# Kernel optimization log

Measured on AMD Instinct MI355X. Metric: run time of the kernel, lower is better.

The kernel has to match this reference:

```python
import jax, jax.numpy as jnp
import numpy as np
from jax.scipy.special import erfinv

N_CHUNKS = 64
D = 128          # input_dim
O = 256          # output_dim
B = 4096         # batch (batch_last)
P = D // 2       # number of 2D pairs

def get_borders_cdf_grid(n):
    # CDF (Gaussian-quantile) spaced grid borders; clip probs to keep endpoints finite
    p = jnp.clip(jnp.arange(n + 1, dtype=jnp.float32) / n, 0.5 / n, 1.0 - 0.5 / n)
    return jnp.sqrt(2.0) * erfinv(2.0 * p - 1.0)

BORDERS = get_borders_cdf_grid(N_CHUNKS)  # (n_chunks+1,)


def setup_inputs() -> dict:
    key = jax.random.key(0)
    ks = jax.random.split(key, 5)
    s = 1.0 / np.sqrt(D)
    return {
        "x": jax.random.normal(ks[0], (D, B), dtype=jnp.float32),
        "weight_lmKAN": jnp.ones((1,), dtype=jnp.float32),
        "apply_relu_linear": 1,
        "func_parameter": jax.random.uniform(ks[1], (N_CHUNKS + 1, N_CHUNKS + 1, O, P), minval=-s, maxval=s, dtype=jnp.float32),
        "scale_parameters": jnp.ones((D,), dtype=jnp.float32),
        "bias_parameters": jnp.zeros((D,), dtype=jnp.float32),
        "W_linear": jax.random.uniform(ks[2], (O, D), minval=-s, maxval=s, dtype=jnp.float32),
        "bias_linear": jax.random.uniform(ks[3], (O,), minval=-s, maxval=s, dtype=jnp.float32),
    }


def lmkan_2d(fp, x):
    """2D bucketized grid lookup + bilinear interpolation.
    fp: (G, G, O, P) with G = n_chunks+1; x: (D, B) -> out (O, B)."""
    n = fp.shape[0] - 1
    pairs = x.reshape(P, 2, -1)                      # adjacent-channel pairs
    eps = 1e-6
    x1 = jnp.clip(pairs[:, 0], BORDERS[0], BORDERS[-1] - eps)  # (P, B)
    x2 = jnp.clip(pairs[:, 1], BORDERS[0], BORDERS[-1] - eps)
    i = jnp.clip(jnp.searchsorted(BORDERS, x1, side='right') - 1, 0, n - 1)
    j = jnp.clip(jnp.searchsorted(BORDERS, x2, side='right') - 1, 0, n - 1)
    t1 = (x1 - BORDERS[i]) / (BORDERS[i + 1] - BORDERS[i])      # (P, B) in [0,1)
    t2 = (x2 - BORDERS[j]) / (BORDERS[j + 1] - BORDERS[j])
    pidx = jnp.arange(P)[:, None]                    # (P, 1) -> broadcasts to (P, B)

    def corner(ii, jj, w):
        g = fp[ii, jj, :, pidx]                      # gather -> (P, B, O)
        return jnp.einsum('pb,pbo->ob', w, g)

    return (corner(i,     j,     (1.0 - t1) * (1.0 - t2))
          + corner(i + 1, j,     t1 * (1.0 - t2))
          + corner(i,     j + 1, (1.0 - t1) * t2)
          + corner(i + 1, j + 1, t1 * t2))


def reference(x, weight_lmKAN, apply_relu_linear, func_parameter, scale_parameters, bias_parameters, W_linear, bias_linear):
    # relu_last=True branch of the original forward
    linear_out = W_linear @ x + bias_linear[:, None]         # (O, B)
    if apply_relu_linear:
        linear_out = jax.nn.relu(linear_out)
    xs = x * scale_parameters[:, None] + bias_parameters[:, None]  # apply_scale / apply_bias
    # apply_tanh=False
    lmkan_out = lmkan_2d(func_parameter, xs)                 # (O, B)
    return 1.0 * linear_out + weight_lmKAN * lmkan_out
```

## Files before the change

### kernel.cpp

```cpp
#include <hip/hip_runtime.h>
#include <hip/hip_fp16.h>


#define NB 4096
#define ND 128
#define NO 256
#define NP 64
#define NG 65
#define PANEL 16384
#define ROW2OFF (64 * 65 * 256)

typedef float f32x4 __attribute__((ext_vector_type(4)));
union Pack8 { __half h[8]; uint4 v; };

__device__ __forceinline__ int bsearch65(const float* B, float v) {
  int lo = 0, hi = 65;
  while (lo < hi) {
    int m = (lo + hi) >> 1;
    if (B[m] <= v) lo = m + 1; else hi = m;
  }
  int i = lo - 1;
  return i < 0 ? 0 : (i > 63 ? 63 : i);
}

__global__ __launch_bounds__(256) void lmkan_transpose2(
    const float* __restrict__ src, __half* __restrict__ dst) {
  const int panel = blockIdx.x;
  const int i = panel / NG, j = panel % NG;
  const int t = threadIdx.x;
  __shared__ __half lds[256 * 72];

  const f32x4* s4 = reinterpret_cast<const f32x4*>(src + (size_t)panel * PANEL);
#pragma unroll
  for (int k = 0; k < 16; ++k) {
    int idx4 = t + 256 * k;
    f32x4 v = __builtin_nontemporal_load(&s4[idx4]);
    int o = idx4 >> 4;
    int p0 = (idx4 & 15) * 4;
    union { __half2 h2[2]; uint2 u; } pk;
    pk.h2[0] = __floats2half2_rn(v[0], v[1]);
    pk.h2[1] = __floats2half2_rn(v[2], v[3]);
    *reinterpret_cast<uint2*>(&lds[o * 72 + p0]) = pk.u;
  }
  __syncthreads();

  const int p = t & 63, oc = t >> 6;
  __half* dbase = dst + (((size_t)(i * 64 + p) * NG + j) * NO) + oc * 64;
#pragma unroll
  for (int s = 0; s < 8; ++s) {
    Pack8 pk;
#pragma unroll
    for (int r = 0; r < 8; ++r) pk.h[r] = lds[(oc * 64 + 8 * s + r) * 72 + p];
    *reinterpret_cast<uint4*>(dbase + 8 * s) = pk.v;
  }
}

__device__ __forceinline__ void fma8(float acc[8], float w, uint4 v) {
  const __half2* h = reinterpret_cast<const __half2*>(&v);
#pragma unroll
  for (int k = 0; k < 4; ++k) {
    float2 f = __half22float2(h[k]);
    acc[2 * k]     = fmaf(w, f.x, acc[2 * k]);
    acc[2 * k + 1] = fmaf(w, f.y, acc[2 * k + 1]);
  }
}

__global__ __launch_bounds__(256) void lmkan_gather4(
    const float* __restrict__ x, const float* __restrict__ scale,
    const float* __restrict__ biasp, const float* __restrict__ wlm_p,
    const __half* __restrict__ fpt, float* __restrict__ out) {
  const int b = blockIdx.x;
  const int t = threadIdx.x;
  const int w = t >> 6;
  const int l = t & 63;
  const int sideJ = l >> 5;
  const int o0 = 8 * (l & 31);

  __shared__ float borders[66];
  __shared__ float xcol[ND];
  __shared__ int pbaseEl[NP];
  __shared__ float2 pws[2][NP];
  __shared__ float lm[4][NO];

  if (t < 65) {
    float pk = fminf(fmaxf((float)t * (1.0f / 64.0f), 0.0078125f), 0.9921875f);
    borders[t] = 1.41421356237309515f * erfinvf(2.0f * pk - 1.0f);
  }
  if (t < ND) xcol[t] = x[(size_t)t * NB + b];
  __syncthreads();

  if (t < NP) {
    const int p = t;
    float x1 = xcol[2 * p]     * scale[2 * p]     + biasp[2 * p];
    float x2 = xcol[2 * p + 1] * scale[2 * p + 1] + biasp[2 * p + 1];
    const float lo = borders[0];
    const float hi = borders[64] - 1e-6f;
    x1 = fminf(fmaxf(x1, lo), hi);
    x2 = fminf(fmaxf(x2, lo), hi);
    int i = bsearch65(borders, x1);
    int j = bsearch65(borders, x2);
    float t1 = (x1 - borders[i]) / (borders[i + 1] - borders[i]);
    float t2 = (x2 - borders[j]) / (borders[j + 1] - borders[j]);
    pbaseEl[p] = ((i * 64 + p) * NG + j) * NO;
    pws[0][p] = make_float2((1.0f - t1) * (1.0f - t2), t1 * (1.0f - t2));
    pws[1][p] = make_float2((1.0f - t1) * t2,          t1 * t2);
  }
  __syncthreads();

  float acc[8] = {0, 0, 0, 0, 0, 0, 0, 0};
  const int p0 = w * 16;
  const int loff = 8 * l;

  const __half* q = fpt + pbaseEl[p0] + loff;
  uint4 v0 = *reinterpret_cast<const uint4*>(q);
  uint4 v1 = *reinterpret_cast<const uint4*>(q + ROW2OFF);
#pragma unroll
  for (int pi = 0; pi < 16; ++pi) {
    const int p = p0 + pi;
    uint4 c0 = v0, c1 = v1;
    if (pi < 15) {
      const __half* qn = fpt + pbaseEl[p + 1] + loff;
      v0 = *reinterpret_cast<const uint4*>(qn);
      v1 = *reinterpret_cast<const uint4*>(qn + ROW2OFF);
    }
    const float2 wv = pws[sideJ][p];
    fma8(acc, wv.x, c0);
    fma8(acc, wv.y, c1);
  }
#pragma unroll
  for (int k = 0; k < 8; ++k) acc[k] += __shfl_xor(acc[k], 32, 64);
  if (l < 32) {
#pragma unroll
    for (int k = 0; k < 8; ++k) lm[w][o0 + k] = acc[k];
  }
  __syncthreads();

  const int o = t;
  float lmsum = lm[0][o] + lm[1][o] + lm[2][o] + lm[3][o];
  out[(size_t)o * NB + b] = wlm_p[0] * lmsum;
}

__global__ __launch_bounds__(256) void lmkan_linear(
    const float* __restrict__ x, const float* __restrict__ W,
    const float* __restrict__ bias_l, const int* __restrict__ relu_p,
    float* __restrict__ out) {
  const int b0 = blockIdx.x * 32;
  const int t = threadIdx.x;
  __shared__ __align__(16) float xs[32 * 132];

#pragma unroll
  for (int k = 0; k < 16; ++k) {
    int idx = t + 256 * k;
    int d = idx >> 5, bb = idx & 31;
    xs[bb * 132 + d] = x[(size_t)d * NB + b0 + bb];
  }
  __syncthreads();

  float acc[32];
#pragma unroll
  for (int bb = 0; bb < 32; ++bb) acc[bb] = 0.0f;

  const float4* W4 = reinterpret_cast<const float4*>(W + (size_t)t * ND);
#pragma unroll 8
  for (int d4 = 0; d4 < 32; ++d4) {
    float4 wv = W4[d4];
#pragma unroll
    for (int bb = 0; bb < 32; ++bb) {
      float4 xv = *reinterpret_cast<const float4*>(&xs[bb * 132 + d4 * 4]);
      acc[bb] = fmaf(wv.x, xv.x, acc[bb]);
      acc[bb] = fmaf(wv.y, xv.y, acc[bb]);
      acc[bb] = fmaf(wv.z, xv.z, acc[bb]);
      acc[bb] = fmaf(wv.w, xv.w, acc[bb]);
    }
  }

  const float bias = bias_l[t];
  const int rl = relu_p[0];
  float* orow = out + (size_t)t * NB + b0;
#pragma unroll
  for (int bb = 0; bb < 32; ++bb) {
    float v = acc[bb] + bias;
    if (rl) v = fmaxf(v, 0.0f);
    orow[bb] += v;
  }
}

__global__ __launch_bounds__(64) void lmkan_gather_direct(
    const float* __restrict__ x, const float* __restrict__ scale,
    const float* __restrict__ biasp, const float* __restrict__ W,
    const float* __restrict__ bias_l, const float* __restrict__ wlm_p,
    const int* __restrict__ relu_p, const float* __restrict__ fp,
    float* __restrict__ out) {
  const int b = blockIdx.x;
  const int t = threadIdx.x;

  __shared__ float borders[66];
  __shared__ __align__(16) float xcol[ND];
  __shared__ int pbase[NP];
  __shared__ float4 pw[NP];

  for (int k = t; k < 65; k += 64) {
    float pk = fminf(fmaxf((float)k * (1.0f / 64.0f), 0.0078125f), 0.9921875f);
    borders[k] = 1.41421356237309515f * erfinvf(2.0f * pk - 1.0f);
  }
  xcol[t]      = x[(size_t)t * NB + b];
  xcol[t + 64] = x[(size_t)(t + 64) * NB + b];
  __syncthreads();

  {
    const int p = t;
    float x1 = xcol[2 * p]     * scale[2 * p]     + biasp[2 * p];
    float x2 = xcol[2 * p + 1] * scale[2 * p + 1] + biasp[2 * p + 1];
    const float lo = borders[0];
    const float hi = borders[64] - 1e-6f;
    x1 = fminf(fmaxf(x1, lo), hi);
    x2 = fminf(fmaxf(x2, lo), hi);
    int i = bsearch65(borders, x1);
    int j = bsearch65(borders, x2);
    float t1 = (x1 - borders[i]) / (borders[i + 1] - borders[i]);
    float t2 = (x2 - borders[j]) / (borders[j + 1] - borders[j]);
    pbase[p] = i * NG + j;
    pw[p] = make_float4((1.0f - t1) * (1.0f - t2), t1 * (1.0f - t2),
                        (1.0f - t1) * t2, t1 * t2);
  }
  __syncthreads();

  float acc[4] = {0, 0, 0, 0};
  for (int p = 0; p < NP; ++p) {
    int base = pbase[p];
    float4 wv = pw[p];
#pragma unroll
    for (int k = 0; k < 4; ++k) {
      size_t r = ((size_t)base * NO + (4 * t + k)) * NP + p;
      acc[k] += wv.x * fp[r] + wv.y * fp[r + 65 * PANEL] +
                wv.z * fp[r + PANEL] + wv.w * fp[r + 66 * PANEL];
    }
  }

  const float wlm = wlm_p[0];
  const int rl = relu_p[0];
  const float4* xc4 = reinterpret_cast<const float4*>(xcol);
#pragma unroll
  for (int k = 0; k < 4; ++k) {
    const int o = 4 * t + k;
    const float4* wr = reinterpret_cast<const float4*>(W + (size_t)o * ND);
    float s = 0.0f;
#pragma unroll 8
    for (int d4 = 0; d4 < ND / 4; ++d4) {
      float4 wv = wr[d4];
      float4 xv = xc4[d4];
      s = fmaf(wv.x, xv.x, s);
      s = fmaf(wv.y, xv.y, s);
      s = fmaf(wv.z, xv.z, s);
      s = fmaf(wv.w, xv.w, s);
    }
    s += bias_l[o];
    if (rl) s = fmaxf(s, 0.0f);
    out[(size_t)o * NB + b] = s + wlm * acc[k];
  }
}

extern "C" void kernel_launch(void* const* d_in, const int* in_sizes, int n_in,
                              void* d_out, int out_size, void* d_ws, size_t ws_size,
                              hipStream_t stream) {
  const float* x     = reinterpret_cast<const float*>(d_in[0]);
  const float* wlm   = reinterpret_cast<const float*>(d_in[1]);
  const int*   relu  = reinterpret_cast<const int*>(d_in[2]);
  const float* fp    = reinterpret_cast<const float*>(d_in[3]);
  const float* scale = reinterpret_cast<const float*>(d_in[4]);
  const float* biasp = reinterpret_cast<const float*>(d_in[5]);
  const float* W     = reinterpret_cast<const float*>(d_in[6]);
  const float* bl    = reinterpret_cast<const float*>(d_in[7]);
  float* out = reinterpret_cast<float*>(d_out);

  const size_t need = (size_t)NG * NG * PANEL * sizeof(__half);
  if (ws_size >= need) {
    __half* fpt = reinterpret_cast<__half*>(d_ws);
    lmkan_transpose2<<<NG * NG, 256, 0, stream>>>(fp, fpt);
    lmkan_gather4<<<NB, 256, 0, stream>>>(x, scale, biasp, wlm, fpt, out);
    lmkan_linear<<<NB / 32, 256, 0, stream>>>(x, W, bl, relu, out);
  } else {
    lmkan_gather_direct<<<NB, 64, 0, stream>>>(x, scale, biasp, W, bl, wlm, relu, fp, out);
  }
}
```

Baseline: 193.6 us.

## Store transposed grid as [i][j][p][o] and gather four corners per lane

The half-precision workspace layout moves from [i][p][j][o] to [i][j][p][o], so each panel is written contiguously. The transpose kernel now writes full 512-byte rows per pair and uses an XOR swizzle on the LDS staging buffer to cut bank conflicts on the strided reads. In the gather kernel each lane now covers 4 outputs and loads all four bilinear corners (at offsets of 0, 1, 65 and 66 panels), which removes the cross-half shuffle reduction. In exchange it issues twice as many narrower 8-byte loads per pair, and the four corners sit in more widely separated memory regions.

Result: faster. 182.4 us (-5.8%).

```diff
diff --git a/kernel.cpp b/kernel.cpp
--- a/kernel.cpp
+++ b/kernel.cpp
@@ -8,7 +8,6 @@
 #define NP 64
 #define NG 65
 #define PANEL 16384
-#define ROW2OFF (64 * 65 * 256)
 
 typedef float f32x4 __attribute__((ext_vector_type(4)));
 union Pack8 { __half h[8]; uint4 v; };
@@ -23,10 +22,9 @@
   return i < 0 ? 0 : (i > 63 ? 63 : i);
 }
 
-__global__ __launch_bounds__(256) void lmkan_transpose2(
+__global__ __launch_bounds__(256) void lmkan_transpose3(
     const float* __restrict__ src, __half* __restrict__ dst) {
   const int panel = blockIdx.x;
-  const int i = panel / NG, j = panel % NG;
   const int t = threadIdx.x;
   __shared__ __half lds[256 * 72];
 
@@ -37,35 +35,40 @@
     f32x4 v = __builtin_nontemporal_load(&s4[idx4]);
     int o = idx4 >> 4;
     int p0 = (idx4 & 15) * 4;
+    int p0s = p0 ^ (((o >> 3) & 15) << 2);
     union { __half2 h2[2]; uint2 u; } pk;
     pk.h2[0] = __floats2half2_rn(v[0], v[1]);
     pk.h2[1] = __floats2half2_rn(v[2], v[3]);
-    *reinterpret_cast<uint2*>(&lds[o * 72 + p0]) = pk.u;
-  }
-  __syncthreads();
-
-  const int p = t & 63, oc = t >> 6;
-  __half* dbase = dst + (((size_t)(i * 64 + p) * NG + j) * NO) + oc * 64;
-#pragma unroll
-  for (int s = 0; s < 8; ++s) {
+    *reinterpret_cast<uint2*>(&lds[o * 72 + p0s]) = pk.u;
+  }
+  __syncthreads();
+
+  const int l = t & 63, w = t >> 6;
+  const int o0 = (l & 31) * 8;
+  const int swz = (l & 15) << 2;
+#pragma unroll
+  for (int ss = 0; ss < 8; ++ss) {
+    int p = ss * 8 + w * 2 + (l >> 5);
+    int prow = ((p & ~3) ^ swz) + (p & 3);
     Pack8 pk;
 #pragma unroll
-    for (int r = 0; r < 8; ++r) pk.h[r] = lds[(oc * 64 + 8 * s + r) * 72 + p];
-    *reinterpret_cast<uint4*>(dbase + 8 * s) = pk.v;
-  }
-}
-
-__device__ __forceinline__ void fma8(float acc[8], float w, uint4 v) {
-  const __half2* h = reinterpret_cast<const __half2*>(&v);
-#pragma unroll
-  for (int k = 0; k < 4; ++k) {
-    float2 f = __half22float2(h[k]);
-    acc[2 * k]     = fmaf(w, f.x, acc[2 * k]);
-    acc[2 * k + 1] = fmaf(w, f.y, acc[2 * k + 1]);
-  }
-}
-
-__global__ __launch_bounds__(256) void lmkan_gather4(
+    for (int r = 0; r < 8; ++r) pk.h[r] = lds[(o0 + r) * 72 + prow];
+    *reinterpret_cast<uint4*>(dst + ((size_t)panel * 64 + p) * NO + o0) = pk.v;
+  }
+}
+
+__device__ __forceinline__ void fma4h(float acc[4], float w, uint2 v) {
+  __half2 h0 = *reinterpret_cast<__half2*>(&v.x);
+  __half2 h1 = *reinterpret_cast<__half2*>(&v.y);
+  float2 f0 = __half22float2(h0);
+  float2 f1 = __half22float2(h1);
+  acc[0] = fmaf(w, f0.x, acc[0]);
+  acc[1] = fmaf(w, f0.y, acc[1]);
+  acc[2] = fmaf(w, f1.x, acc[2]);
+  acc[3] = fmaf(w, f1.y, acc[3]);
+}
+
+__global__ __launch_bounds__(256) void lmkan_gather5(
     const float* __restrict__ x, const float* __restrict__ scale,
     const float* __restrict__ biasp, const float* __restrict__ wlm_p,
     const __half* __restrict__ fpt, float* __restrict__ out) {
@@ -73,14 +76,12 @@
   const int t = threadIdx.x;
   const int w = t >> 6;
   const int l = t & 63;
-  const int sideJ = l >> 5;
-  const int o0 = 8 * (l & 31);
 
   __shared__ float borders[66];
   __shared__ float xcol[ND];
   __shared__ int pbaseEl[NP];
-  __shared__ float2 pws[2][NP];
-  __shared__ float lm[4][NO];
+  __shared__ float4 pw[NP];
+  __shared__ __align__(16) float lm[4][NO];
 
   if (t < 65) {
     float pk = fminf(fmaxf((float)t * (1.0f / 64.0f), 0.0078125f), 0.9921875f);
@@ -101,38 +102,42 @@
     int j = bsearch65(borders, x2);
     float t1 = (x1 - borders[i]) / (borders[i + 1] - borders[i]);
     float t2 = (x2 - borders[j]) / (borders[j + 1] - borders[j]);
-    pbaseEl[p] = ((i * 64 + p) * NG + j) * NO;
-    pws[0][p] = make_float2((1.0f - t1) * (1.0f - t2), t1 * (1.0f - t2));
-    pws[1][p] = make_float2((1.0f - t1) * t2,          t1 * t2);
-  }
-  __syncthreads();
-
-  float acc[8] = {0, 0, 0, 0, 0, 0, 0, 0};
+    pbaseEl[p] = ((i * NG + j) * 64 + p) * NO;
+    pw[p] = make_float4((1.0f - t1) * (1.0f - t2),
+                        (1.0f - t1) * t2,
+                        t1 * (1.0f - t2),
+                        t1 * t2);
+  }
+  __syncthreads();
+
+  float acc[4] = {0, 0, 0, 0};
   const int p0 = w * 16;
-  const int loff = 8 * l;
+  const int loff = 4 * l;
 
   const __half* q = fpt + pbaseEl[p0] + loff;
-  uint4 v0 = *reinterpret_cast<const uint4*>(q);
-  uint4 v1 = *reinterpret_cast<const uint4*>(q + ROW2OFF);
+  uint2 vA = *reinterpret_cast<const uint2*>(q);
+  uint2 vB = *reinterpret_cast<const uint2*>(q + PANEL);
+  uint2 vC = *reinterpret_cast<const uint2*>(q + 65 * PANEL);
+  uint2 vD = *reinterpret_cast<const uint2*>(q + 66 * PANEL);
 #pragma unroll
   for (int pi = 0; pi < 16; ++pi) {
     const int p = p0 + pi;
-    uint4 c0 = v0, c1 = v1;
+    uint2 cA = vA, cB = vB, cC = vC, cD = vD;
     if (pi < 15) {
       const __half* qn = fpt + pbaseEl[p + 1] + loff;
-      v0 = *reinterpret_cast<const uint4*>(qn);
-      v1 = *reinterpret_cast<const uint4*>(qn + ROW2OFF);
-    }
-    const float2 wv = pws[sideJ][p];
-    fma8(acc, wv.x, c0);
-    fma8(acc, wv.y, c1);
-  }
-#pragma unroll
-  for (int k = 0; k < 8; ++k) acc[k] += __shfl_xor(acc[k], 32, 64);
-  if (l < 32) {
-#pragma unroll
-    for (int k = 0; k < 8; ++k) lm[w][o0 + k] = acc[k];
-  }
+      vA = *reinterpret_cast<const uint2*>(qn);
+      vB = *reinterpret_cast<const uint2*>(qn + PANEL);
+      vC = *reinterpret_cast<const uint2*>(qn + 65 * PANEL);
+      vD = *reinterpret_cast<const uint2*>(qn + 66 * PANEL);
+    }
+    const float4 wv = pw[p];
+    fma4h(acc, wv.x, cA);
+    fma4h(acc, wv.y, cB);
+    fma4h(acc, wv.z, cC);
+    fma4h(acc, wv.w, cD);
+  }
+  *reinterpret_cast<float4*>(&lm[w][loff]) =
+      make_float4(acc[0], acc[1], acc[2], acc[3]);
   __syncthreads();
 
   const int o = t;
@@ -276,8 +281,8 @@
   const size_t need = (size_t)NG * NG * PANEL * sizeof(__half);
   if (ws_size >= need) {
     __half* fpt = reinterpret_cast<__half*>(d_ws);
-    lmkan_transpose2<<<NG * NG, 256, 0, stream>>>(fp, fpt);
-    lmkan_gather4<<<NB, 256, 0, stream>>>(x, scale, biasp, wlm, fpt, out);
+    lmkan_transpose3<<<NG * NG, 256, 0, stream>>>(fp, fpt);
+    lmkan_gather5<<<NB, 256, 0, stream>>>(x, scale, biasp, wlm, fpt, out);
     lmkan_linear<<<NB / 32, 256, 0, stream>>>(x, W, bl, relu, out);
   } else {
     lmkan_gather_direct<<<NB, 64, 0, stream>>>(x, scale, biasp, W, bl, wlm, relu, fp, out);
```

## Reorder fp16 table to pair-major slabs and swizzle transpose LDS

Applied to the files above, without the earlier changes.

The transposed fp16 parameter table changes from (i,p,j,o) ordering to a pair-major (p,i,j,o) layout. Each pair's data now sits in one contiguous slab, and the i+1 corner is a short NG*NO offset away instead of a far row offset. The transpose kernel also XOR-swizzles its LDS writes and reads to cut bank conflicts, and its global writes now go to the new layout. The goal is better locality for the gather and a cheaper transpose. The cost is scattered writes across slabs during the transpose.

Result: faster. 184.7 us (-4.6%).

```diff
diff --git a/kernel.cpp b/kernel.cpp
--- a/kernel.cpp
+++ b/kernel.cpp
@@ -7,8 +7,11 @@
 #define NO 256
 #define NP 64
 #define NG 65
+#define NPANEL 4225
 #define PANEL 16384
-#define ROW2OFF (64 * 65 * 256)
+#define SLAB_ELEMS ((size_t)NPANEL * NO)
+#define FPT_ELEMS ((size_t)NP * SLAB_ELEMS)
+#define FPT_BYTES (FPT_ELEMS * 2)
 
 typedef float f32x4 __attribute__((ext_vector_type(4)));
 union Pack8 { __half h[8]; uint4 v; };
@@ -23,10 +26,16 @@
   return i < 0 ? 0 : (i > 63 ? 63 : i);
 }
 
-__global__ __launch_bounds__(256) void lmkan_transpose2(
+__device__ __forceinline__ void borders_init(float* borders, int t) {
+  if (t < 65) {
+    float pk = fminf(fmaxf((float)t * (1.0f / 64.0f), 0.0078125f), 0.9921875f);
+    borders[t] = 1.41421356237309515f * erfinvf(2.0f * pk - 1.0f);
+  }
+}
+
+__global__ __launch_bounds__(256) void lmkan_transpose4(
     const float* __restrict__ src, __half* __restrict__ dst) {
   const int panel = blockIdx.x;
-  const int i = panel / NG, j = panel % NG;
   const int t = threadIdx.x;
   __shared__ __half lds[256 * 72];
 
@@ -37,21 +46,25 @@
     f32x4 v = __builtin_nontemporal_load(&s4[idx4]);
     int o = idx4 >> 4;
     int p0 = (idx4 & 15) * 4;
+    int p0s = p0 ^ (((o >> 3) & 15) << 2);
     union { __half2 h2[2]; uint2 u; } pk;
     pk.h2[0] = __floats2half2_rn(v[0], v[1]);
     pk.h2[1] = __floats2half2_rn(v[2], v[3]);
-    *reinterpret_cast<uint2*>(&lds[o * 72 + p0]) = pk.u;
-  }
-  __syncthreads();
-
-  const int p = t & 63, oc = t >> 6;
-  __half* dbase = dst + (((size_t)(i * 64 + p) * NG + j) * NO) + oc * 64;
-#pragma unroll
-  for (int s = 0; s < 8; ++s) {
+    *reinterpret_cast<uint2*>(&lds[o * 72 + p0s]) = pk.u;
+  }
+  __syncthreads();
+
+  const int l = t & 63, w = t >> 6;
+  const int o0 = (l & 31) * 8;
+  const int swz = (l & 15) << 2;
+#pragma unroll
+  for (int ss = 0; ss < 8; ++ss) {
+    int p = ss * 8 + w * 2 + (l >> 5);
+    int prow = ((p & ~3) ^ swz) + (p & 3);
     Pack8 pk;
 #pragma unroll
-    for (int r = 0; r < 8; ++r) pk.h[r] = lds[(oc * 64 + 8 * s + r) * 72 + p];
-    *reinterpret_cast<uint4*>(dbase + 8 * s) = pk.v;
+    for (int r = 0; r < 8; ++r) pk.h[r] = lds[(o0 + r) * 72 + prow];
+    *reinterpret_cast<uint4*>(dst + ((size_t)p * NPANEL + panel) * NO + o0) = pk.v;
   }
 }
 
@@ -65,7 +78,7 @@
   }
 }
 
-__global__ __launch_bounds__(256) void lmkan_gather4(
+__global__ __launch_bounds__(256) void lmkan_gather11(
     const float* __restrict__ x, const float* __restrict__ scale,
     const float* __restrict__ biasp, const float* __restrict__ wlm_p,
     const __half* __restrict__ fpt, float* __restrict__ out) {
@@ -73,19 +86,17 @@
   const int t = threadIdx.x;
   const int w = t >> 6;
   const int l = t & 63;
-  const int sideJ = l >> 5;
-  const int o0 = 8 * (l & 31);
+  const int side = l >> 5;
+  const int ol = l & 31;
+  const int loff = 8 * l;
 
   __shared__ float borders[66];
   __shared__ float xcol[ND];
-  __shared__ int pbaseEl[NP];
+  __shared__ int jb[NP];
   __shared__ float2 pws[2][NP];
-  __shared__ float lm[4][NO];
-
-  if (t < 65) {
-    float pk = fminf(fmaxf((float)t * (1.0f / 64.0f), 0.0078125f), 0.9921875f);
-    borders[t] = 1.41421356237309515f * erfinvf(2.0f * pk - 1.0f);
-  }
+  __shared__ __align__(16) float lm[4][NO];
+
+  borders_init(borders, t);
   if (t < ND) xcol[t] = x[(size_t)t * NB + b];
   __syncthreads();
 
@@ -101,29 +112,30 @@
     int j = bsearch65(borders, x2);
     float t1 = (x1 - borders[i]) / (borders[i + 1] - borders[i]);
     float t2 = (x2 - borders[j]) / (borders[j + 1] - borders[j]);
-    pbaseEl[p] = ((i * 64 + p) * NG + j) * NO;
-    pws[0][p] = make_float2((1.0f - t1) * (1.0f - t2), t1 * (1.0f - t2));
-    pws[1][p] = make_float2((1.0f - t1) * t2,          t1 * t2);
+    jb[p] = (p * NPANEL + i * NG + j) * NO;
+    pws[0][p] = make_float2((1.0f - t1) * (1.0f - t2),
+                            t1 * (1.0f - t2));
+    pws[1][p] = make_float2((1.0f - t1) * t2,
+                            t1 * t2);
   }
   __syncthreads();
 
   float acc[8] = {0, 0, 0, 0, 0, 0, 0, 0};
   const int p0 = w * 16;
-  const int loff = 8 * l;
-
-  const __half* q = fpt + pbaseEl[p0] + loff;
+
+  const __half* q = fpt + jb[p0] + loff;
   uint4 v0 = *reinterpret_cast<const uint4*>(q);
-  uint4 v1 = *reinterpret_cast<const uint4*>(q + ROW2OFF);
+  uint4 v1 = *reinterpret_cast<const uint4*>(q + NG * NO);
 #pragma unroll
   for (int pi = 0; pi < 16; ++pi) {
     const int p = p0 + pi;
     uint4 c0 = v0, c1 = v1;
     if (pi < 15) {
-      const __half* qn = fpt + pbaseEl[p + 1] + loff;
+      const __half* qn = fpt + jb[p + 1] + loff;
       v0 = *reinterpret_cast<const uint4*>(qn);
-      v1 = *reinterpret_cast<const uint4*>(qn + ROW2OFF);
-    }
-    const float2 wv = pws[sideJ][p];
+      v1 = *reinterpret_cast<const uint4*>(qn + NG * NO);
+    }
+    const float2 wv = pws[side][p];
     fma8(acc, wv.x, c0);
     fma8(acc, wv.y, c1);
   }
@@ -131,13 +143,13 @@
   for (int k = 0; k < 8; ++k) acc[k] += __shfl_xor(acc[k], 32, 64);
   if (l < 32) {
 #pragma unroll
-    for (int k = 0; k < 8; ++k) lm[w][o0 + k] = acc[k];
+    for (int k = 0; k < 8; ++k) lm[w][8 * ol + k] = acc[k];
   }
   __syncthreads();
 
   const int o = t;
-  float lmsum = lm[0][o] + lm[1][o] + lm[2][o] + lm[3][o];
-  out[(size_t)o * NB + b] = wlm_p[0] * lmsum;
+  out[(size_t)o * NB + b] =
+      wlm_p[0] * (lm[0][o] + lm[1][o] + lm[2][o] + lm[3][o]);
 }
 
 __global__ __launch_bounds__(256) void lmkan_linear(
@@ -273,11 +285,10 @@
   const float* bl    = reinterpret_cast<const float*>(d_in[7]);
   float* out = reinterpret_cast<float*>(d_out);
 
-  const size_t need = (size_t)NG * NG * PANEL * sizeof(__half);
-  if (ws_size >= need) {
+  if (ws_size >= FPT_BYTES) {
     __half* fpt = reinterpret_cast<__half*>(d_ws);
-    lmkan_transpose2<<<NG * NG, 256, 0, stream>>>(fp, fpt);
-    lmkan_gather4<<<NB, 256, 0, stream>>>(x, scale, biasp, wlm, fpt, out);
+    lmkan_transpose4<<<NPANEL, 256, 0, stream>>>(fp, fpt);
+    lmkan_gather11<<<NB, 256, 0, stream>>>(x, scale, biasp, wlm, fpt, out);
     lmkan_linear<<<NB / 32, 256, 0, stream>>>(x, W, bl, relu, out);
   } else {
     lmkan_gather_direct<<<NB, 64, 0, stream>>>(x, scale, biasp, W, bl, wlm, relu, fp, out);
```
